# Performance work log

Measured on AMD Instinct MI355X. Metric: run time of the kernel, lower is better.

The kernel has to match this reference:

```python
import jax, jax.numpy as jnp
import numpy as np

B = 256   # number of segments
P = 2000  # points per segment (hard-coded by fc_1 = Linear(2000*32, 1024))
C = 32    # point feature channels
EPS_BN = 1e-5


def _bn_relu(h, g, b):
    # BatchNorm1d in training mode: batch statistics over axis 0, biased variance.
    m = jnp.mean(h, axis=0)
    v = jnp.var(h, axis=0)
    return jax.nn.relu((h - m) * jax.lax.rsqrt(v + EPS_BN) * g + b)


def setup_inputs() -> dict:
    key = jax.random.key(0)
    ks = jax.random.split(key, 16)
    s = 0.02
    inp = {
        "x": jax.random.normal(ks[0], (B * P, C), jnp.float32),
        "length": jnp.full((B,), P, dtype=jnp.int32),
        # attention MLP (1x1 conv1d chain 32->16->8->1), torch layout [out,in]
        "w1": jax.random.normal(ks[1], (16, 32), jnp.float32) * s,
        "b1": jnp.zeros((16,), jnp.float32),
        "g1": jnp.ones((16,), jnp.float32),
        "be1": jnp.zeros((16,), jnp.float32),
        "w2": jax.random.normal(ks[2], (8, 16), jnp.float32) * s,
        "b2": jnp.zeros((8,), jnp.float32),
        "g2": jnp.ones((8,), jnp.float32),
        "be2": jnp.zeros((8,), jnp.float32),
        "w3": jax.random.normal(ks[3], (1, 8), jnp.float32) * s,
        "b3": jnp.zeros((1,), jnp.float32),
        "g3": jnp.ones((1,), jnp.float32),
        "be3": jnp.zeros((1,), jnp.float32),
        # FC head
        "fw1": jax.random.normal(ks[4], (1024, P * C), jnp.float32) * s,
        "fb1": jnp.zeros((1024,), jnp.float32),
        "fg1": jnp.ones((1024,), jnp.float32),
        "fbe1": jnp.zeros((1024,), jnp.float32),
        "fw2": jax.random.normal(ks[5], (256, 1024), jnp.float32) * s,
        "fb2": jnp.zeros((256,), jnp.float32),
        "fg2": jnp.ones((256,), jnp.float32),
        "fbe2": jnp.zeros((256,), jnp.float32),
    }
    return inp


def reference(x, length, w1, b1, g1, be1, w2, b2, g2, be2, w3, b3, g3, be3,
              fw1, fb1, fg1, fbe1, fw2, fb2, fg2, fbe2):
    # Pointwise attention score MLP over all points (BN stats over the full
    # point dimension, matching conv1d+BatchNorm1d with batch size 1).
    h = _bn_relu(x @ w1.T + b1, g1, be1)          # [N,16]
    h = _bn_relu(h @ w2.T + b2, g2, be2)          # [N,8]
    score = _bn_relu(h @ w3.T + b3, g3, be3)      # [N,1]

    # Per-segment softmax over the point dim, then weighted features + flatten.
    # All segments have exactly P=2000 points (required by fc_1's input dim),
    # so the ragged slicing collapses to a dense [B,P,*] reshape.
    att = jax.nn.softmax(score.reshape(B, P, 1), axis=1)   # [B,P,1]
    pooled = (x.reshape(B, P, C) * att).reshape(B, P * C)  # [B,64000]

    r = _bn_relu(pooled @ fw1.T + fb1, fg1, fbe1)  # [B,1024]
    r = _bn_relu(r @ fw2.T + fb2, fg2, fbe2)       # [B,256]

    # F.normalize(p=2, dim=1, eps=1e-12)
    norm = jnp.maximum(jnp.linalg.norm(r, axis=1, keepdims=True), 1e-12)
    return r / norm
```

## Files before the change

kernel.cpp:

```cpp
#include <hip/hip_runtime.h>
#include <hip/hip_bf16.h>

#define NPTS   512000
#define BSEG   256
#define PSEG   2000
#define CIN    32
#define INV_N  (1.0f/512000.0f)
#define EPS_BN 1e-5f

using u32 = unsigned int;
using u16 = unsigned short;
using f32x4  = __attribute__((ext_vector_type(4))) float;
using bf16x8 = __attribute__((ext_vector_type(8))) short;

static __device__ __forceinline__ u16 f2bf(float f) {
    u32 u = __builtin_bit_cast(u32, f);
    u += 0x7fffu + ((u >> 16) & 1u);
    return (u16)(u >> 16);
}

__global__ __launch_bounds__(256) void k_zero(float4* __restrict__ p) {
    p[blockIdx.x * 256 + threadIdx.x] = float4{0.0f, 0.0f, 0.0f, 0.0f};
}

__global__ __launch_bounds__(256) void k_mlp1(const float* __restrict__ x,
                                              const float* __restrict__ w1,
                                              float* __restrict__ a1,
                                              float* __restrict__ stats) {
    __shared__ float w[512];
    __shared__ float part[4][32];
    const int t = threadIdx.x;
    w[t] = w1[t]; w[t + 256] = w1[t + 256];
    __syncthreads();

    const int idx = blockIdx.x * 256 + t;
    const float4* xr = (const float4*)(x + (size_t)idx * 32);
    float4 xv[8];
#pragma unroll
    for (int i = 0; i < 8; i++) xv[i] = xr[i];

    float h[16];
#pragma unroll
    for (int c = 0; c < 16; c++) {
        float s = 0.0f;
        const float4* wr = (const float4*)(w + c * 32);
#pragma unroll
        for (int i = 0; i < 8; i++) {
            float4 wv = wr[i];
            s += xv[i].x * wv.x + xv[i].y * wv.y + xv[i].z * wv.z + xv[i].w * wv.w;
        }
        h[c] = s;
    }

    float4* ar = (float4*)(a1 + (size_t)idx * 16);
#pragma unroll
    for (int i = 0; i < 4; i++) {
        float4 o; o.x = h[i*4+0]; o.y = h[i*4+1]; o.z = h[i*4+2]; o.w = h[i*4+3];
        ar[i] = o;
    }

    const int lane = t & 63, wave = t >> 6;
#pragma unroll
    for (int c = 0; c < 16; c++) {
        float s = h[c], q = h[c] * h[c];
#pragma unroll
        for (int off = 32; off > 0; off >>= 1) {
            s += __shfl_down(s, off);
            q += __shfl_down(q, off);
        }
        if (lane == 0) { part[wave][c] = s; part[wave][16 + c] = q; }
    }
    __syncthreads();
    if (t < 32) {
        float tot = part[0][t] + part[1][t] + part[2][t] + part[3][t];
        atomicAdd(&stats[t], tot);
    }
}

__global__ __launch_bounds__(256) void k_mlp2(const float* __restrict__ a1,
                                              const float* __restrict__ w2,
                                              const float* __restrict__ g1,
                                              const float* __restrict__ be1,
                                              float* __restrict__ a2,
                                              float* __restrict__ stats) {
    __shared__ float w[128];
    __shared__ float sc[16], sh[16];
    __shared__ float part[4][16];
    const int t = threadIdx.x;
    if (t < 128) w[t] = w2[t];
    if (t < 16) {
        float m = stats[t] * INV_N;
        float v = stats[16 + t] * INV_N - m * m;
        float s = g1[t] * rsqrtf(v + EPS_BN);
        sc[t] = s; sh[t] = be1[t] - m * s;
    }
    __syncthreads();

    const int idx = blockIdx.x * 256 + t;
    const float4* ar = (const float4*)(a1 + (size_t)idx * 16);
    float h[16];
#pragma unroll
    for (int i = 0; i < 4; i++) {
        float4 v4 = ar[i];
        h[i*4+0] = v4.x; h[i*4+1] = v4.y; h[i*4+2] = v4.z; h[i*4+3] = v4.w;
    }
#pragma unroll
    for (int c = 0; c < 16; c++) h[c] = fmaxf(fmaf(h[c], sc[c], sh[c]), 0.0f);

    float o[8];
#pragma unroll
    for (int c = 0; c < 8; c++) {
        float s = 0.0f;
#pragma unroll
        for (int k = 0; k < 16; k++) s += h[k] * w[c * 16 + k];
        o[c] = s;
    }
    float4* orp = (float4*)(a2 + (size_t)idx * 8);
    float4 o0; o0.x=o[0]; o0.y=o[1]; o0.z=o[2]; o0.w=o[3];
    float4 o1; o1.x=o[4]; o1.y=o[5]; o1.z=o[6]; o1.w=o[7];
    orp[0] = o0; orp[1] = o1;

    const int lane = t & 63, wave = t >> 6;
#pragma unroll
    for (int c = 0; c < 8; c++) {
        float s = o[c], q = o[c] * o[c];
#pragma unroll
        for (int off = 32; off > 0; off >>= 1) {
            s += __shfl_down(s, off);
            q += __shfl_down(q, off);
        }
        if (lane == 0) { part[wave][c] = s; part[wave][8 + c] = q; }
    }
    __syncthreads();
    if (t < 16) {
        float tot = part[0][t] + part[1][t] + part[2][t] + part[3][t];
        atomicAdd(&stats[32 + t], tot);
    }
}

__global__ __launch_bounds__(256) void k_mlp3(const float* __restrict__ a2,
                                              const float* __restrict__ w3,
                                              const float* __restrict__ g2,
                                              const float* __restrict__ be2,
                                              float* __restrict__ a3,
                                              float* __restrict__ stats) {
    __shared__ float w[8], sc[8], sh[8];
    __shared__ float part[4][2];
    const int t = threadIdx.x;
    if (t < 8) {
        w[t] = w3[t];
        float m = stats[32 + t] * INV_N;
        float v = stats[40 + t] * INV_N - m * m;
        float s = g2[t] * rsqrtf(v + EPS_BN);
        sc[t] = s; sh[t] = be2[t] - m * s;
    }
    __syncthreads();

    const int idx = blockIdx.x * 256 + t;
    const float4* ar = (const float4*)(a2 + (size_t)idx * 8);
    float4 v0 = ar[0], v1 = ar[1];
    float h[8] = {v0.x, v0.y, v0.z, v0.w, v1.x, v1.y, v1.z, v1.w};
    float s = 0.0f;
#pragma unroll
    for (int c = 0; c < 8; c++) s += fmaxf(fmaf(h[c], sc[c], sh[c]), 0.0f) * w[c];
    a3[idx] = s;

    const int lane = t & 63, wave = t >> 6;
    float q = s * s;
    float ss = s;
#pragma unroll
    for (int off = 32; off > 0; off >>= 1) {
        ss += __shfl_down(ss, off);
        q  += __shfl_down(q, off);
    }
    if (lane == 0) { part[wave][0] = ss; part[wave][1] = q; }
    __syncthreads();
    if (t < 2) {
        float tot = part[0][t] + part[1][t] + part[2][t] + part[3][t];
        atomicAdd(&stats[48 + t], tot);
    }
}

__global__ __launch_bounds__(256) void k_pool(const float* __restrict__ a3,
                                              const float* __restrict__ x,
                                              const float* __restrict__ g3,
                                              const float* __restrict__ be3,
                                              const float* __restrict__ stats,
                                              u16* __restrict__ pooled) {
    const int b = blockIdx.x, t = threadIdx.x;
    const float m  = stats[48] * INV_N;
    const float v  = stats[49] * INV_N - m * m;
    const float sc = g3[0] * rsqrtf(v + EPS_BN);
    const float sh = be3[0] - m * sc;

    float sv[8];
    float mx = -1e30f;
#pragma unroll
    for (int i = 0; i < 8; i++) {
        int p = t + i * 256;
        if (p < PSEG) {
            float val = fmaxf(fmaf(a3[(size_t)b * PSEG + p], sc, sh), 0.0f);
            sv[i] = val; mx = fmaxf(mx, val);
        } else sv[i] = -1e30f;
    }
    const int lane = t & 63, wave = t >> 6;
    __shared__ float redm[4], reds[4];
#pragma unroll
    for (int off = 32; off > 0; off >>= 1) mx = fmaxf(mx, __shfl_xor(mx, off));
    if (lane == 0) redm[wave] = mx;
    __syncthreads();
    mx = fmaxf(fmaxf(redm[0], redm[1]), fmaxf(redm[2], redm[3]));

    float es = 0.0f;
#pragma unroll
    for (int i = 0; i < 8; i++) {
        int p = t + i * 256;
        if (p < PSEG) { float e = __expf(sv[i] - mx); sv[i] = e; es += e; }
    }
#pragma unroll
    for (int off = 32; off > 0; off >>= 1) es += __shfl_xor(es, off);
    if (lane == 0) reds[wave] = es;
    __syncthreads();
    const float inv = 1.0f / (reds[0] + reds[1] + reds[2] + reds[3]);

#pragma unroll
    for (int i = 0; i < 8; i++) {
        int p = t + i * 256;
        if (p >= PSEG) continue;
        const float att = sv[i] * inv;
        const float4* xr = (const float4*)(x + ((size_t)b * PSEG + p) * 32);
        u16* dst = pooled + (size_t)b * 64000 + (size_t)p * 32;
#pragma unroll
        for (int u = 0; u < 4; u++) {
            float4 f0 = xr[u * 2], f1 = xr[u * 2 + 1];
            u32 q0 = (u32)f2bf(f0.x * att) | ((u32)f2bf(f0.y * att) << 16);
            u32 q1 = (u32)f2bf(f0.z * att) | ((u32)f2bf(f0.w * att) << 16);
            u32 q2 = (u32)f2bf(f1.x * att) | ((u32)f2bf(f1.y * att) << 16);
            u32 q3 = (u32)f2bf(f1.z * att) | ((u32)f2bf(f1.w * att) << 16);
            uint4 q; q.x = q0; q.y = q1; q.z = q2; q.w = q3;
            *(uint4*)(dst + u * 8) = q;
        }
    }
}

__global__ __launch_bounds__(256) void k_gemm4(const u16* __restrict__ pooled,
                                               const float* __restrict__ fw1,
                                               float* __restrict__ a4) {
    __shared__ alignas(16) char smem[40960];
    char* As = smem;
    char* Bs = smem + 32768;

    const int t = threadIdx.x;
    const int jblk = blockIdx.x;
    const int kblk = blockIdx.y;
    const int wave = t >> 6, lane = t & 63;
    const int kbase = kblk * 1600;

    f32x4 acc[4][4] = {};

    for (int step = 0; step < 25; ++step) {
        const int k0 = kbase + step * 64;
        {
            const int r  = t >> 3;
            const int ks = (t & 7) * 8;
#pragma unroll
            for (int i = 0; i < 8; i++) {
                const int row = i * 32 + r;
                uint4 v = *(const uint4*)(pooled + (size_t)row * 64000 + k0 + ks);
                const int byte = (row * 128 + ks * 2) ^ ((row & 7) << 4);
                *(uint4*)(As + byte) = v;
            }
        }
        {
            const int jj = t >> 4;
            const int ks = (t & 15) * 4;
#pragma unroll
            for (int i = 0; i < 4; i++) {
                const int j = i * 16 + jj;
                float4 v = *(const float4*)(fw1 + (size_t)(jblk * 64 + j) * 64000 + k0 + ks);
                ushort4 bv;
                bv.x = f2bf(v.x); bv.y = f2bf(v.y); bv.z = f2bf(v.z); bv.w = f2bf(v.w);
                const int byte = (j * 128 + ks * 2) ^ ((j & 7) << 4);
                *(ushort4*)(Bs + byte) = bv;
            }
        }
        __syncthreads();
#pragma unroll
        for (int kk = 0; kk < 2; ++kk) {
            const int krow = kk * 32 + (lane >> 4) * 8;
            bf16x8 aF[4], bF[4];
#pragma unroll
            for (int mm = 0; mm < 4; mm++) {
                const int row = wave * 64 + mm * 16 + (lane & 15);
                aF[mm] = *(const bf16x8*)(As + ((row * 128 + krow * 2) ^ ((row & 7) << 4)));
            }
#pragma unroll
            for (int nn = 0; nn < 4; nn++) {
                const int col = nn * 16 + (lane & 15);
                bF[nn] = *(const bf16x8*)(Bs + ((col * 128 + krow * 2) ^ ((col & 7) << 4)));
            }
#pragma unroll
            for (int mm = 0; mm < 4; mm++)
#pragma unroll
                for (int nn = 0; nn < 4; nn++)
                    acc[mm][nn] = __builtin_amdgcn_mfma_f32_16x16x32_bf16(
                        aF[mm], bF[nn], acc[mm][nn], 0, 0, 0);
        }
        __syncthreads();
    }

#pragma unroll
    for (int mm = 0; mm < 4; mm++)
#pragma unroll
        for (int nn = 0; nn < 4; nn++)
#pragma unroll
            for (int r = 0; r < 4; r++) {
                const int row = wave * 64 + mm * 16 + (lane >> 4) * 4 + r;
                const int col = jblk * 64 + nn * 16 + (lane & 15);
                atomicAdd(&a4[(size_t)row * 1024 + col], acc[mm][nn][r]);
            }
}

__global__ __launch_bounds__(256) void k_bn4stats(const float* __restrict__ a4,
                                                  float* __restrict__ stats) {
    __shared__ float ps[4][64], pq[4][64];
    const int t = threadIdx.x;
    const int c  = (blockIdx.x << 6) + (t & 63);
    const int rq = t >> 6;
    float s = 0.0f, q = 0.0f;
#pragma unroll 8
    for (int i = rq * 64; i < rq * 64 + 64; i++) {
        float v = a4[(size_t)i * 1024 + c];
        s += v; q += v * v;
    }
    ps[rq][t & 63] = s; pq[rq][t & 63] = q;
    __syncthreads();
    if (rq == 0) {
        float ts = ps[0][t] + ps[1][t] + ps[2][t] + ps[3][t];
        float tq = pq[0][t] + pq[1][t] + pq[2][t] + pq[3][t];
        stats[64 + c] = ts; stats[1088 + c] = tq;
    }
}

__global__ __launch_bounds__(256) void k_fc2(const float* __restrict__ a4,
                                             const float* __restrict__ fg1,
                                             const float* __restrict__ fbe1,
                                             const float* __restrict__ fw2,
                                             float* __restrict__ stats,
                                             float* __restrict__ a5) {
    __shared__ alignas(16) float h[1024];
    const int i = blockIdx.x, t = threadIdx.x;
#pragma unroll
    for (int u = 0; u < 4; u++) {
        const int k = u * 256 + t;
        float m  = stats[64 + k] * (1.0f / 256.0f);
        float v  = stats[1088 + k] * (1.0f / 256.0f) - m * m;
        float sc = fg1[k] * rsqrtf(v + EPS_BN);
        float sh = fbe1[k] - m * sc;
        h[k] = fmaxf(fmaf(a4[(size_t)i * 1024 + k], sc, sh), 0.0f);
    }
    __syncthreads();
    const float4* wr = (const float4*)(fw2 + (size_t)t * 1024);
    const float4* hr = (const float4*)h;
    float s = 0.0f;
#pragma unroll 4
    for (int u = 0; u < 256; u++) {
        float4 w = wr[u], hv = hr[u];
        s += w.x * hv.x + w.y * hv.y + w.z * hv.z + w.w * hv.w;
    }
    a5[(size_t)i * 256 + t] = s;
    atomicAdd(&stats[2112 + t], s);
    atomicAdd(&stats[2368 + t], s * s);
}

__global__ __launch_bounds__(256) void k_norm(const float* __restrict__ a5,
                                              const float* __restrict__ fg2,
                                              const float* __restrict__ fbe2,
                                              const float* __restrict__ stats,
                                              float* __restrict__ out) {
    const int i = blockIdx.x, t = threadIdx.x;
    float m  = stats[2112 + t] * (1.0f / 256.0f);
    float v  = stats[2368 + t] * (1.0f / 256.0f) - m * m;
    float sc = fg2[t] * rsqrtf(v + EPS_BN);
    float sh = fbe2[t] - m * sc;
    float r = fmaxf(fmaf(a5[(size_t)i * 256 + t], sc, sh), 0.0f);

    float q = r * r;
    const int lane = t & 63, wave = t >> 6;
#pragma unroll
    for (int off = 32; off > 0; off >>= 1) q += __shfl_xor(q, off);
    __shared__ float red[4];
    if (lane == 0) red[wave] = q;
    __syncthreads();
    float tot = red[0] + red[1] + red[2] + red[3];
    float nrm = fmaxf(sqrtf(tot), 1e-12f);
    out[(size_t)i * 256 + t] = r / nrm;
}

extern "C" void kernel_launch(void* const* d_in, const int* in_sizes, int n_in,
                              void* d_out, int out_size, void* d_ws, size_t ws_size,
                              hipStream_t stream) {
    const float* x   = (const float*)d_in[0];
    const float* w1  = (const float*)d_in[2];
    const float* g1  = (const float*)d_in[4];
    const float* be1 = (const float*)d_in[5];
    const float* w2  = (const float*)d_in[6];
    const float* g2  = (const float*)d_in[8];
    const float* be2 = (const float*)d_in[9];
    const float* w3  = (const float*)d_in[10];
    const float* g3  = (const float*)d_in[12];
    const float* be3 = (const float*)d_in[13];
    const float* fw1 = (const float*)d_in[14];
    const float* fg1 = (const float*)d_in[16];
    const float* fbe1= (const float*)d_in[17];
    const float* fw2 = (const float*)d_in[18];
    const float* fg2 = (const float*)d_in[20];
    const float* fbe2= (const float*)d_in[21];
    float* out = (float*)d_out;

    char* ws = (char*)d_ws;
    float* stats = (float*)ws;
    float* a4 = (float*)(ws + 16384);
    float* a5 = (float*)(ws + 16384 + 1048576);
    char*  big = ws + 16384 + 1048576 + 262144;
    float* a1 = (float*)big;
    u16*   pooled = (u16*)big;
    float* a2 = (float*)(big + 32768000);
    float* a3 = (float*)(big + 32768000 + 16384000);

    k_zero<<<260, 256, 0, stream>>>((float4*)ws);
    k_mlp1<<<2000, 256, 0, stream>>>(x, w1, a1, stats);
    k_mlp2<<<2000, 256, 0, stream>>>(a1, w2, g1, be1, a2, stats);
    k_mlp3<<<2000, 256, 0, stream>>>(a2, w3, g2, be2, a3, stats);
    k_pool<<<256, 256, 0, stream>>>(a3, x, g3, be3, stats, pooled);
    k_gemm4<<<dim3(16, 40), 256, 0, stream>>>(pooled, fw1, a4);
    k_bn4stats<<<16, 256, 0, stream>>>(a4, stats);
    k_fc2<<<256, 256, 0, stream>>>(a4, fg1, fbe1, fw2, stats, a5);
    k_norm<<<256, 256, 0, stream>>>(a5, fg2, fbe2, stats, out);
}
```

Before: 325.9 us.

## Load pooled tiles via direct global-to-LDS and replace split-K atomics with partial buffers

k_pool now writes the pooled bf16 matrix in a pre-swizzled layout, so k_gemm4 can fill its A tile with direct global-to-LDS loads (global_load_lds) instead of staging through registers. The split-K atomicAdd epilogue is replaced by plain stores into per-K-block partial buffers. A new k_red4 kernel sums the 40 partials, writes a4, and accumulates the BN statistics with atomics. This removes contended float atomics and register staging, at the cost of a 40 MB partial buffer being written and then read back.

New measurement: 334.3 us. +2.6%, slower.

```diff
diff --git a/kernel.cpp b/kernel.cpp
--- a/kernel.cpp
+++ b/kernel.cpp
@@ -17,6 +17,12 @@
     u32 u = __builtin_bit_cast(u32, f);
     u += 0x7fffu + ((u >> 16) & 1u);
     return (u16)(u >> 16);
+}
+
+static __device__ __forceinline__ void gload_lds16(const void* g, void* l) {
+    __builtin_amdgcn_global_load_lds(
+        (const __attribute__((address_space(1))) unsigned int*)g,
+        (__attribute__((address_space(3))) unsigned int*)l, 16, 0, 0);
 }
 
 __global__ __launch_bounds__(256) void k_zero(float4* __restrict__ p) {
@@ -223,13 +229,15 @@
     __syncthreads();
     const float inv = 1.0f / (reds[0] + reds[1] + reds[2] + reds[3]);
 
+    const int swz = (b & 7) << 3;
 #pragma unroll
     for (int i = 0; i < 8; i++) {
         int p = t + i * 256;
         if (p >= PSEG) continue;
         const float att = sv[i] * inv;
         const float4* xr = (const float4*)(x + ((size_t)b * PSEG + p) * 32);
-        u16* dst = pooled + (size_t)b * 64000 + (size_t)p * 32;
+        u16* dst = pooled + (size_t)b * 64000 + (size_t)(p >> 1) * 64;
+        const int half = (p & 1) << 5;
 #pragma unroll
         for (int u = 0; u < 4; u++) {
             float4 f0 = xr[u * 2], f1 = xr[u * 2 + 1];
@@ -238,14 +246,14 @@
             u32 q2 = (u32)f2bf(f1.x * att) | ((u32)f2bf(f1.y * att) << 16);
             u32 q3 = (u32)f2bf(f1.z * att) | ((u32)f2bf(f1.w * att) << 16);
             uint4 q; q.x = q0; q.y = q1; q.z = q2; q.w = q3;
-            *(uint4*)(dst + u * 8) = q;
+            *(uint4*)(dst + ((half | (u << 3)) ^ swz)) = q;
         }
     }
 }
 
 __global__ __launch_bounds__(256) void k_gemm4(const u16* __restrict__ pooled,
                                                const float* __restrict__ fw1,
-                                               float* __restrict__ a4) {
+                                               float* __restrict__ a4p) {
     __shared__ alignas(16) char smem[40960];
     char* As = smem;
     char* Bs = smem + 32768;
@@ -261,15 +269,12 @@
     for (int step = 0; step < 25; ++step) {
         const int k0 = kbase + step * 64;
         {
-            const int r  = t >> 3;
-            const int ks = (t & 7) * 8;
-#pragma unroll
-            for (int i = 0; i < 8; i++) {
-                const int row = i * 32 + r;
-                uint4 v = *(const uint4*)(pooled + (size_t)row * 64000 + k0 + ks);
-                const int byte = (row * 128 + ks * 2) ^ ((row & 7) << 4);
-                *(uint4*)(As + byte) = v;
-            }
+            const u16* gs = pooled + (size_t)(wave * 8 + (lane >> 3)) * 64000
+                            + k0 + (lane & 7) * 8;
+            char* ld = As + wave * 1024;
+#pragma unroll
+            for (int i = 0; i < 8; i++)
+                gload_lds16(gs + (size_t)i * 32 * 64000, ld + i * 4096);
         }
         {
             const int jj = t >> 4;
@@ -309,6 +314,7 @@
         __syncthreads();
     }
 
+    float* dst = a4p + (size_t)kblk * 262144;
 #pragma unroll
     for (int mm = 0; mm < 4; mm++)
 #pragma unroll
@@ -317,29 +323,30 @@
             for (int r = 0; r < 4; r++) {
                 const int row = wave * 64 + mm * 16 + (lane >> 4) * 4 + r;
                 const int col = jblk * 64 + nn * 16 + (lane & 15);
-                atomicAdd(&a4[(size_t)row * 1024 + col], acc[mm][nn][r]);
+                dst[(size_t)row * 1024 + col] = acc[mm][nn][r];
             }
 }
 
-__global__ __launch_bounds__(256) void k_bn4stats(const float* __restrict__ a4,
-                                                  float* __restrict__ stats) {
-    __shared__ float ps[4][64], pq[4][64];
-    const int t = threadIdx.x;
-    const int c  = (blockIdx.x << 6) + (t & 63);
-    const int rq = t >> 6;
-    float s = 0.0f, q = 0.0f;
+__global__ __launch_bounds__(256) void k_red4(const float* __restrict__ a4p,
+                                              float* __restrict__ a4,
+                                              float* __restrict__ stats) {
+    const int i = blockIdx.x, t = threadIdx.x;
+    float4 s = {0.0f, 0.0f, 0.0f, 0.0f};
 #pragma unroll 8
-    for (int i = rq * 64; i < rq * 64 + 64; i++) {
-        float v = a4[(size_t)i * 1024 + c];
-        s += v; q += v * v;
-    }
-    ps[rq][t & 63] = s; pq[rq][t & 63] = q;
-    __syncthreads();
-    if (rq == 0) {
-        float ts = ps[0][t] + ps[1][t] + ps[2][t] + ps[3][t];
-        float tq = pq[0][t] + pq[1][t] + pq[2][t] + pq[3][t];
-        stats[64 + c] = ts; stats[1088 + c] = tq;
-    }
+    for (int kb = 0; kb < 40; kb++) {
+        float4 v = *(const float4*)(a4p + (size_t)kb * 262144 + (size_t)i * 1024 + t * 4);
+        s.x += v.x; s.y += v.y; s.z += v.z; s.w += v.w;
+    }
+    *(float4*)(a4 + (size_t)i * 1024 + t * 4) = s;
+    const int j = t * 4;
+    atomicAdd(&stats[64 + j + 0], s.x);
+    atomicAdd(&stats[64 + j + 1], s.y);
+    atomicAdd(&stats[64 + j + 2], s.z);
+    atomicAdd(&stats[64 + j + 3], s.w);
+    atomicAdd(&stats[1088 + j + 0], s.x * s.x);
+    atomicAdd(&stats[1088 + j + 1], s.y * s.y);
+    atomicAdd(&stats[1088 + j + 2], s.z * s.z);
+    atomicAdd(&stats[1088 + j + 3], s.w * s.w);
 }
 
 __global__ __launch_bounds__(256) void k_fc2(const float* __restrict__ a4,
@@ -422,19 +429,20 @@
     float* stats = (float*)ws;
     float* a4 = (float*)(ws + 16384);
     float* a5 = (float*)(ws + 16384 + 1048576);
-    char*  big = ws + 16384 + 1048576 + 262144;
+    float* a4p = (float*)(ws + 16384 + 1048576 + 262144);
+    char*  big = ws + 16384 + 1048576 + 262144 + 41943040;
     float* a1 = (float*)big;
     u16*   pooled = (u16*)big;
     float* a2 = (float*)(big + 32768000);
     float* a3 = (float*)(big + 32768000 + 16384000);
 
-    k_zero<<<260, 256, 0, stream>>>((float4*)ws);
+    k_zero<<<4, 256, 0, stream>>>((float4*)ws);
     k_mlp1<<<2000, 256, 0, stream>>>(x, w1, a1, stats);
     k_mlp2<<<2000, 256, 0, stream>>>(a1, w2, g1, be1, a2, stats);
     k_mlp3<<<2000, 256, 0, stream>>>(a2, w3, g2, be2, a3, stats);
     k_pool<<<256, 256, 0, stream>>>(a3, x, g3, be3, stats, pooled);
-    k_gemm4<<<dim3(16, 40), 256, 0, stream>>>(pooled, fw1, a4);
-    k_bn4stats<<<16, 256, 0, stream>>>(a4, stats);
+    k_gemm4<<<dim3(16, 40), 256, 0, stream>>>(pooled, fw1, a4p);
+    k_red4<<<256, 256, 0, stream>>>(a4p, a4, stats);
     k_fc2<<<256, 256, 0, stream>>>(a4, fg1, fbe1, fw2, stats, a5);
     k_norm<<<256, 256, 0, stream>>>(a5, fg2, fbe2, stats, out);
 }
```
